# Performance work log

Measured on AMD Instinct MI355X. Metric: run time of the kernel, lower is better.

Reference implementation:

```python
import jax, jax.numpy as jnp
import numpy as np

# SequentialEdge (torchdrug): for each offset i in [-D, D], connect every atom of
# residue r to every atom of residue r+i within the same graph, keep only pairs on
# the same chain, relation id = i + D. We use a regular batch (B graphs, R residues
# per graph, A atoms per residue) so all shapes are static; edges filtered out by
# the same-chain test are padded with -1 rows (the torch original compacts them,
# which is a data-dependent shape and not jit-expressible).

B, R, A, D = 256, 256, 8, 2  # graphs, residues/graph, atoms/residue, max_distance
N = B * R * A
RTOT = B * R


def setup_inputs() -> dict:
    key = jax.random.key(0)
    atom2residue = jnp.arange(N, dtype=jnp.int32) // A        # [N]
    residue2graph = jnp.arange(RTOT, dtype=jnp.int32) // R    # [RTOT]
    chain_id = jax.random.randint(key, (RTOT,), 0, 4, dtype=jnp.int32)  # 4 chains/graph
    return {
        "chain_id": chain_id,
        "atom2residue": atom2residue,
        "residue2graph": residue2graph,
        "num_graph": B,
        "residues_per_graph": R,
        "atoms_per_residue": A,
        "max_distance": D,
    }


def reference(chain_id, atom2residue, residue2graph, num_graph, residues_per_graph,
              atoms_per_residue, max_distance):
    Bg, Rr, Aa, Dd = num_graph, residues_per_graph, atoms_per_residue, max_distance
    a = jnp.arange(Aa, dtype=jnp.int32)
    g = jnp.arange(Bg, dtype=jnp.int32)
    chunks = []
    for i in range(-Dd, Dd + 1):  # small fixed loop over 2*D+1 relation offsets
        Rv = Rr - abs(i)
        lo = max(0, -i)  # first valid local residue index for node_in
        local_in = jnp.arange(lo, lo + Rv, dtype=jnp.int32)           # [Rv]
        res_in = g[:, None] * Rr + local_in[None, :]                   # [B, Rv] global residue ids
        res_out = res_in + i                                           # partner residue, same graph
        node_in = res_in[..., None] * Aa + a                           # [B, Rv, A]
        node_out = res_out[..., None] * Aa + a                         # [B, Rv, A]
        # variadic_meshgrid order: in-atom varies slowly, out-atom fast, per residue segment
        ni = jnp.broadcast_to(node_in[..., :, None], (Bg, Rv, Aa, Aa)).reshape(-1)
        no = jnp.broadcast_to(node_out[..., None, :], (Bg, Rv, Aa, Aa)).reshape(-1)
        same_chain = chain_id[atom2residue[ni]] == chain_id[atom2residue[no]]
        rel = jnp.full(ni.shape, i + Dd, dtype=jnp.int32)
        edges = jnp.stack([ni, no, rel], axis=-1)                      # [E_i, 3]
        chunks.append(jnp.where(same_chain[:, None], edges, jnp.int32(-1)))
    edge_list = jnp.concatenate(chunks, axis=0)                        # [E_total, 3]
    return edge_list, jnp.int32(2 * Dd + 1)
```

## Files before the change

kernel.cpp:

```cpp
#include <hip/hip_runtime.h>
#include <hip/hip_bf16.h>


#define E_TOTAL   20873216u
#define INT_TOTAL 62619648u
#define NT4       15654912u

__device__ __forceinline__ void decode_edge(unsigned e, const int* __restrict__ ch,
                                            int& x, int& y, int& z) {
    unsigned g, rem;
    int i, lo, rel;
    if (e < 4161536u) {
        unsigned eo = e;
        g = eo / 16256u; rem = eo - g * 16256u; i = -2; lo = 2; rel = 0;
    } else if (e < 8339456u) {
        unsigned eo = e - 4161536u;
        g = eo / 16320u; rem = eo - g * 16320u; i = -1; lo = 1; rel = 1;
    } else if (e < 12533760u) {
        unsigned eo = e - 8339456u;
        g = eo >> 14;    rem = eo & 16383u;     i = 0;  lo = 0; rel = 2;
    } else if (e < 16711680u) {
        unsigned eo = e - 12533760u;
        g = eo / 16320u; rem = eo - g * 16320u; i = 1;  lo = 0; rel = 3;
    } else {
        unsigned eo = e - 16711680u;
        g = eo / 16256u; rem = eo - g * 16256u; i = 2;  lo = 0; rel = 4;
    }
    unsigned rl = (rem >> 6) + (unsigned)lo;
    unsigned ai = (rem >> 3) & 7u;
    unsigned ao = rem & 7u;
    int res_in  = (int)(g * 256u + rl);
    int res_out = res_in + i;
    bool same = (ch[res_in] == ch[res_out]);
    x = same ? res_in  * 8 + (int)ai : -1;
    y = same ? res_out * 8 + (int)ao : -1;
    z = same ? rel : -1;
}

__global__ __launch_bounds__(256)
void seqedge_kernel(const int* __restrict__ chain, int* __restrict__ out) {
    unsigned t = blockIdx.x * 256u + threadIdx.x;
    if (t >= NT4) return;
    unsigned j0 = t * 4u;
    unsigned e0 = j0 / 3u;
    unsigned c0 = j0 - e0 * 3u;
    unsigned e1 = e0 + 1u;
    if (e1 >= E_TOTAL) e1 = E_TOTAL - 1u;

    int x0, y0, z0, x1, y1, z1;
    decode_edge(e0, chain, x0, y0, z0);
    decode_edge(e1, chain, x1, y1, z1);

    int4 v;
    if (c0 == 0u)      v = make_int4(x0, y0, z0, x1);
    else if (c0 == 1u) v = make_int4(y0, z0, x1, y1);
    else               v = make_int4(z0, x1, y1, z1);

    reinterpret_cast<int4*>(out)[t] = v;

    if (t == 0u) out[INT_TOTAL] = 5;
}

extern "C" void kernel_launch(void* const* d_in, const int* in_sizes, int n_in,
                              void* d_out, int out_size, void* d_ws, size_t ws_size,
                              hipStream_t stream) {
    const int* chain_id = (const int*)d_in[0];
    int* out = (int*)d_out;
    const unsigned nthreads = NT4;
    const unsigned nblocks = (nthreads + 255u) / 256u;
    seqedge_kernel<<<nblocks, 256, 0, stream>>>(chain_id, out);
}
```

Before: 251.3 us.

## Decode four edges per thread and stage through padded LDS for coalesced stores

Each thread now decodes one group of four consecutive edges that share an input atom, so the segment decode and the two chain lookups happen once per four edges instead of twice per int4 of output. The twelve output ints per thread are written into shared memory with a padded layout, then the block re-reads them and emits contiguous int4 stores. This cuts redundant index arithmetic and global loads in a write-bound kernel. It adds a block barrier and LDS traffic, and relies on 4-edge groups never straddling a segment boundary and on the block count exactly covering E_TOTAL.

Result: no change. 251.6 us (+0.1%).

```diff
diff --git a/kernel.cpp b/kernel.cpp
--- a/kernel.cpp
+++ b/kernel.cpp
@@ -4,61 +4,56 @@
 
 #define E_TOTAL   20873216u
 #define INT_TOTAL 62619648u
-#define NT4       15654912u
-
-__device__ __forceinline__ void decode_edge(unsigned e, const int* __restrict__ ch,
-                                            int& x, int& y, int& z) {
-    unsigned g, rem;
-    int i, lo, rel;
-    if (e < 4161536u) {
-        unsigned eo = e;
-        g = eo / 16256u; rem = eo - g * 16256u; i = -2; lo = 2; rel = 0;
-    } else if (e < 8339456u) {
-        unsigned eo = e - 4161536u;
-        g = eo / 16320u; rem = eo - g * 16320u; i = -1; lo = 1; rel = 1;
-    } else if (e < 12533760u) {
-        unsigned eo = e - 8339456u;
-        g = eo >> 14;    rem = eo & 16383u;     i = 0;  lo = 0; rel = 2;
-    } else if (e < 16711680u) {
-        unsigned eo = e - 12533760u;
-        g = eo / 16320u; rem = eo - g * 16320u; i = 1;  lo = 0; rel = 3;
-    } else {
-        unsigned eo = e - 16711680u;
-        g = eo / 16256u; rem = eo - g * 16256u; i = 2;  lo = 0; rel = 4;
-    }
-    unsigned rl = (rem >> 6) + (unsigned)lo;
-    unsigned ai = (rem >> 3) & 7u;
-    unsigned ao = rem & 7u;
-    int res_in  = (int)(g * 256u + rl);
-    int res_out = res_in + i;
-    bool same = (ch[res_in] == ch[res_out]);
-    x = same ? res_in  * 8 + (int)ai : -1;
-    y = same ? res_out * 8 + (int)ao : -1;
-    z = same ? rel : -1;
-}
 
 __global__ __launch_bounds__(256)
 void seqedge_kernel(const int* __restrict__ chain, int* __restrict__ out) {
-    unsigned t = blockIdx.x * 256u + threadIdx.x;
-    if (t >= NT4) return;
-    unsigned j0 = t * 4u;
-    unsigned e0 = j0 / 3u;
-    unsigned c0 = j0 - e0 * 3u;
-    unsigned e1 = e0 + 1u;
-    if (e1 >= E_TOTAL) e1 = E_TOTAL - 1u;
+    __shared__ int lds[3200];
+    const unsigned tid = threadIdx.x;
+    const unsigned gid = blockIdx.x * 256u + tid;
+    const unsigned e0  = gid * 4u;
 
-    int x0, y0, z0, x1, y1, z1;
-    decode_edge(e0, chain, x0, y0, z0);
-    decode_edge(e1, chain, x1, y1, z1);
+    unsigned g, rem; int i, lo, rel;
+    if (e0 < 4161536u)       { g = e0 / 16256u;                    rem = e0 - g * 16256u; i = -2; lo = 2; rel = 0; }
+    else if (e0 < 8339456u)  { unsigned eo = e0 - 4161536u;  g = eo / 16320u; rem = eo - g * 16320u; i = -1; lo = 1; rel = 1; }
+    else if (e0 < 12533760u) { unsigned eo = e0 - 8339456u;  g = eo >> 14;    rem = eo & 16383u;     i = 0;  lo = 0; rel = 2; }
+    else if (e0 < 16711680u) { unsigned eo = e0 - 12533760u; g = eo / 16320u; rem = eo - g * 16320u; i = 1;  lo = 0; rel = 3; }
+    else                     { unsigned eo = e0 - 16711680u; g = eo / 16256u; rem = eo - g * 16256u; i = 2;  lo = 0; rel = 4; }
 
-    int4 v;
-    if (c0 == 0u)      v = make_int4(x0, y0, z0, x1);
-    else if (c0 == 1u) v = make_int4(y0, z0, x1, y1);
-    else               v = make_int4(z0, x1, y1, z1);
+    const unsigned rl  = (rem >> 6) + (unsigned)lo;
+    const unsigned ai  = (rem >> 3) & 7u;
+    const unsigned ao0 = rem & 7u;
+    const int res_in  = (int)(g * 256u + rl);
+    const int res_out = res_in + i;
+    const bool same = chain[res_in] == chain[res_out];
 
-    reinterpret_cast<int4*>(out)[t] = v;
+    const int x  = same ? res_in * 8 + (int)ai : -1;
+    const int r  = same ? rel : -1;
+    const int yb = res_out * 8 + (int)ao0;
+    const int y0 = same ? yb     : -1;
+    const int y1 = same ? yb + 1 : -1;
+    const int y2 = same ? yb + 2 : -1;
+    const int y3 = same ? yb + 3 : -1;
 
-    if (t == 0u) out[INT_TOTAL] = 5;
+    const unsigned wbase = 12u * tid + 16u * (tid >> 5) + 4u * ((tid >> 3) & 3u);
+    int4* ldsv = reinterpret_cast<int4*>(&lds[wbase]);
+    ldsv[0] = make_int4(x,  y0, r,  x);
+    ldsv[1] = make_int4(y1, r,  x,  y2);
+    ldsv[2] = make_int4(r,  x,  y3, r);
+
+    __syncthreads();
+
+    const unsigned out_base = blockIdx.x * 768u;
+    int4* outv = reinterpret_cast<int4*>(out);
+    #pragma unroll
+    for (unsigned s = 0; s < 3; ++s) {
+        const unsigned m    = s * 256u + tid;
+        const unsigned c    = m / 3u;
+        const unsigned rsub = m - c * 3u;
+        const unsigned pb   = 12u * c + 16u * (c >> 5) + 4u * ((c >> 3) & 3u) + 4u * rsub;
+        outv[out_base + m] = *reinterpret_cast<const int4*>(&lds[pb]);
+    }
+
+    if (gid == 0u) out[INT_TOTAL] = 5;
 }
 
 extern "C" void kernel_launch(void* const* d_in, const int* in_sizes, int n_in,
@@ -66,7 +61,5 @@
                               hipStream_t stream) {
     const int* chain_id = (const int*)d_in[0];
     int* out = (int*)d_out;
-    const unsigned nthreads = NT4;
-    const unsigned nblocks = (nthreads + 255u) / 256u;
-    seqedge_kernel<<<nblocks, 256, 0, stream>>>(chain_id, out);
+    seqedge_kernel<<<20384, 256, 0, stream>>>(chain_id, out);
 }
```
